# Optimization experiments

Hardware: AMD Instinct MI355X
Metric: run time of the kernel (lower is better)

Reference implementation:

```python
import jax, jax.numpy as jnp
import numpy as np

DIM = 512
HEADS = 8
DIM_HEAD = 64
INNER = HEADS * DIM_HEAD  # 512
EPS_LN = 1e-5
EPS_Q = 1e-6


def ternary_quant(w):
    # BitNet-style ternary quantization: scale by mean |w|, round to {-1,0,1}
    s = jnp.mean(jnp.abs(w))
    return jnp.round(jnp.clip(w / (s + EPS_Q), -1.0, 1.0)) * s


def layernorm(x, g, b):
    mu = jnp.mean(x, axis=-1, keepdims=True)
    var = jnp.mean(jnp.square(x - mu), axis=-1, keepdims=True)
    return (x - mu) * jax.lax.rsqrt(var + EPS_LN) * g + b


def setup_inputs() -> dict:
    key = jax.random.key(0)
    ks = jax.random.split(key, 6)
    x = jax.random.normal(ks[0], (8, 1024, DIM), dtype=jnp.float32)
    W_qkv = jax.random.normal(ks[1], (3 * INNER, DIM), dtype=jnp.float32) * (DIM ** -0.5)
    W_out = jax.random.normal(ks[2], (DIM, INNER), dtype=jnp.float32) * (INNER ** -0.5)
    b_out = jnp.zeros((DIM,), dtype=jnp.float32)
    g1 = jnp.ones((DIM,), dtype=jnp.float32)
    b1 = jnp.zeros((DIM,), dtype=jnp.float32)
    g2 = jnp.ones((INNER,), dtype=jnp.float32)
    b2 = jnp.zeros((INNER,), dtype=jnp.float32)
    return {"x": x, "g1": g1, "b1": b1, "W_qkv": W_qkv, "g2": g2, "b2": b2, "W_out": W_out, "b_out": b_out}


def reference(x, g1, b1, W_qkv, g2, b2, W_out, b_out):
    b, n, _ = x.shape
    scale = DIM_HEAD ** -0.5
    x = layernorm(x, g1, b1)
    qkv = x @ ternary_quant(W_qkv).T  # [b, n, 3*inner]
    q, k, v = jnp.split(qkv, 3, axis=-1)
    # b n (h d) -> b h n d
    def split_heads(t):
        return t.reshape(b, n, HEADS, DIM_HEAD).transpose(0, 2, 1, 3)
    q, k, v = split_heads(q), split_heads(k), split_heads(v)
    attn_map = jnp.einsum('bhnd,bhmd->bhnm', q, k) * scale  # [b,h,n,n]
    attn = jax.nn.softmax(attn_map, axis=-1)
    out = jnp.einsum('bhnm,bhmd->bhnd', attn, v)
    out = out.transpose(0, 2, 1, 3).reshape(b, n, INNER)  # b n (h d)
    out = layernorm(out, g2, b2)
    out = out @ ternary_quant(W_out).T + b_out
    return out
```

## Files before the change

### kernel.cpp

```cpp
#include <hip/hip_runtime.h>
#include <hip/hip_bf16.h>

typedef __bf16 bf16x8 __attribute__((ext_vector_type(8)));
typedef float  f32x4  __attribute__((ext_vector_type(4)));

#define SEQ   1024
#define BATCH 8
#define DIMM  512
#define HEADS 8
#define DHEAD 64
#define TRIPLE 1536
#define MROWS (BATCH*SEQ)

#define GLOAD_LDS16(g, l) __builtin_amdgcn_global_load_lds( \
    (const __attribute__((address_space(1))) void*)(const void*)(g), \
    (__attribute__((address_space(3))) void*)(void*)(l), 16, 0, 0)

__global__ __launch_bounds__(256) void absum_all(const float* __restrict__ w1,
                                                 const float* __restrict__ w2,
                                                 float* __restrict__ part) {
    const int bid = blockIdx.x, tid = threadIdx.x;
    float s = 0.f;
    if (bid < 256) {
        const float4* p = (const float4*)w1;
        for (int i = bid * 256 + tid; i < 196608; i += 65536) {
            float4 v = p[i];
            s += fabsf(v.x) + fabsf(v.y) + fabsf(v.z) + fabsf(v.w);
        }
    } else {
        const float4* p = (const float4*)w2;
        for (int i = (bid - 256) * 256 + tid; i < 65536; i += 16384) {
            float4 v = p[i];
            s += fabsf(v.x) + fabsf(v.y) + fabsf(v.z) + fabsf(v.w);
        }
    }
    for (int o = 32; o; o >>= 1) s += __shfl_down(s, o);
    __shared__ float red[4];
    if (!(tid & 63)) red[tid >> 6] = s;
    __syncthreads();
    if (tid == 0) part[bid] = red[0] + red[1] + red[2] + red[3];
}

__global__ __launch_bounds__(256) void quant_all(const float* __restrict__ w1,
                                                 const float* __restrict__ w2,
                                                 const float* __restrict__ part,
                                                 __bf16* __restrict__ o1,
                                                 __bf16* __restrict__ o2) {
    const int bid = blockIdx.x, tid = threadIdx.x;
    float acc = 0.f;
    if (bid < 768) acc = part[tid];
    else if (tid < 64) acc = part[256 + tid];
    for (int o = 32; o; o >>= 1) acc += __shfl_down(acc, o);
    __shared__ float red[4];
    if (!(tid & 63)) red[tid >> 6] = acc;
    __syncthreads();
    const float tot = red[0] + red[1] + red[2] + red[3];
    const float s = (bid < 768) ? tot / 786432.0f : tot / 262144.0f;
    const float inv = 1.f / (s + 1e-6f);

    const float* w; __bf16* o; int idx;
    if (bid < 768) { w = w1; o = o1; idx = (bid * 256 + tid) * 4; }
    else           { w = w2; o = o2; idx = ((bid - 768) * 256 + tid) * 4; }
    float4 v = *reinterpret_cast<const float4*>(w + idx);
    o[idx + 0] = (__bf16)(rintf(fminf(1.f, fmaxf(-1.f, v.x * inv))) * s);
    o[idx + 1] = (__bf16)(rintf(fminf(1.f, fmaxf(-1.f, v.y * inv))) * s);
    o[idx + 2] = (__bf16)(rintf(fminf(1.f, fmaxf(-1.f, v.z * inv))) * s);
    o[idx + 3] = (__bf16)(rintf(fminf(1.f, fmaxf(-1.f, v.w * inv))) * s);
}

template<typename TIN>
__global__ __launch_bounds__(256) void ln_fast(const TIN* __restrict__ x,
                                               const float* __restrict__ g,
                                               const float* __restrict__ bta,
                                               __bf16* __restrict__ y) {
    const int row = blockIdx.x * 4 + (threadIdx.x >> 6);
    const int lane = threadIdx.x & 63;
    float v[8];
    if constexpr (sizeof(TIN) == 4) {
        const float4* xr = (const float4*)((const float*)x + (size_t)row * DIMM + lane * 8);
        float4 a = xr[0], bq = xr[1];
        v[0] = a.x; v[1] = a.y; v[2] = a.z; v[3] = a.w;
        v[4] = bq.x; v[5] = bq.y; v[6] = bq.z; v[7] = bq.w;
    } else {
        bf16x8 a = *reinterpret_cast<const bf16x8*>((const __bf16*)x + (size_t)row * DIMM + lane * 8);
#pragma unroll
        for (int e = 0; e < 8; ++e) v[e] = (float)a[e];
    }
    float s = 0.f, sq = 0.f;
#pragma unroll
    for (int e = 0; e < 8; ++e) { s += v[e]; sq += v[e] * v[e]; }
    for (int o = 32; o; o >>= 1) { s += __shfl_xor(s, o); sq += __shfl_xor(sq, o); }
    const float mu = s * (1.f / DIMM);
    const float invs = rsqrtf(sq * (1.f / DIMM) - mu * mu + 1e-5f);
    const float4* gp = (const float4*)(g + lane * 8);
    const float4* bp = (const float4*)(bta + lane * 8);
    float4 g0 = gp[0], g1 = gp[1], b0 = bp[0], b1 = bp[1];
    float o_[8] = {
        (v[0] - mu) * invs * g0.x + b0.x, (v[1] - mu) * invs * g0.y + b0.y,
        (v[2] - mu) * invs * g0.z + b0.z, (v[3] - mu) * invs * g0.w + b0.w,
        (v[4] - mu) * invs * g1.x + b1.x, (v[5] - mu) * invs * g1.y + b1.y,
        (v[6] - mu) * invs * g1.z + b1.z, (v[7] - mu) * invs * g1.w + b1.w };
    uint4 st;
    asm("v_cvt_pk_bf16_f32 %0, %1, %2" : "=v"(st.x) : "v"(o_[0]), "v"(o_[1]));
    asm("v_cvt_pk_bf16_f32 %0, %1, %2" : "=v"(st.y) : "v"(o_[2]), "v"(o_[3]));
    asm("v_cvt_pk_bf16_f32 %0, %1, %2" : "=v"(st.z) : "v"(o_[4]), "v"(o_[5]));
    asm("v_cvt_pk_bf16_f32 %0, %1, %2" : "=v"(st.w) : "v"(o_[6]), "v"(o_[7]));
    *reinterpret_cast<uint4*>(y + (size_t)row * DIMM + lane * 8) = st;
}

template<int NCOLS, bool BIAS, bool OUT_F32>
__global__ __launch_bounds__(256) void gemm_lds(const __bf16* __restrict__ A,
                                                const __bf16* __restrict__ Wt,
                                                const float* __restrict__ bias,
                                                __bf16* __restrict__ outb,
                                                float* __restrict__ outf) {
    const int K = DIMM;
    __shared__ __align__(16) __bf16 As[2][4096];
    __shared__ __align__(16) __bf16 Bs[2][4096];

    const int tid = threadIdx.x;
    const int w = tid >> 6, lane = tid & 63;
    const int m = lane & 15, g = lane >> 4;
    const int mi = w >> 1, ni = w & 1;

    const int trow = tid >> 2;
    const int tc = tid & 3;
    const int sc = (tc ^ ((trow >> 1) & 3)) * 8;
    const __bf16* a0 = A  + (size_t)(blockIdx.x * 128 + trow) * K + sc;
    const __bf16* a1 = a0 + (size_t)64 * K;
    const __bf16* b0 = Wt + (size_t)(blockIdx.y * 128 + trow) * K + sc;
    const __bf16* b1 = b0 + (size_t)64 * K;

    f32x4 acc[4][4] = {};

    GLOAD_LDS16(a0, (char*)As[0] + tid * 16);
    GLOAD_LDS16(a1, (char*)As[0] + 4096 + tid * 16);
    GLOAD_LDS16(b0, (char*)Bs[0] + tid * 16);
    GLOAD_LDS16(b1, (char*)Bs[0] + 4096 + tid * 16);

    int cur = 0;
    for (int k0 = 0; k0 < K; k0 += 32) {
        __syncthreads();
        if (k0 + 32 < K) {
            GLOAD_LDS16(a0 + k0 + 32, (char*)As[cur ^ 1] + tid * 16);
            GLOAD_LDS16(a1 + k0 + 32, (char*)As[cur ^ 1] + 4096 + tid * 16);
            GLOAD_LDS16(b0 + k0 + 32, (char*)Bs[cur ^ 1] + tid * 16);
            GLOAD_LDS16(b1 + k0 + 32, (char*)Bs[cur ^ 1] + 4096 + tid * 16);
        }

        const char* Ab = (const char*)As[cur];
        const char* Bb = (const char*)Bs[cur];
        bf16x8 af[4], bfr[4];
#pragma unroll
        for (int i = 0; i < 4; ++i) {
            const int ra = mi * 64 + i * 16 + m;
            af[i] = *reinterpret_cast<const bf16x8*>(Ab + ra * 64 + ((g ^ ((ra >> 1) & 3)) << 4));
        }
#pragma unroll
        for (int j = 0; j < 4; ++j) {
            const int rb = ni * 64 + j * 16 + m;
            bfr[j] = *reinterpret_cast<const bf16x8*>(Bb + rb * 64 + ((g ^ ((rb >> 1) & 3)) << 4));
        }
#pragma unroll
        for (int i = 0; i < 4; ++i)
#pragma unroll
            for (int j = 0; j < 4; ++j)
                acc[i][j] = __builtin_amdgcn_mfma_f32_16x16x32_bf16(af[i], bfr[j], acc[i][j], 0, 0, 0);
        cur ^= 1;
    }

    const int orow0 = blockIdx.x * 128 + mi * 64 + g * 4;
    const int ocol0 = blockIdx.y * 128 + ni * 64;
#pragma unroll
    for (int i = 0; i < 4; ++i)
#pragma unroll
        for (int j = 0; j < 4; ++j)
#pragma unroll
            for (int r = 0; r < 4; ++r) {
                int row = orow0 + i * 16 + r;
                int col = ocol0 + j * 16 + m;
                float v = acc[i][j][r];
                if (BIAS) v += bias[col];
                if (OUT_F32) outf[(size_t)row * NCOLS + col] = v;
                else         outb[(size_t)row * NCOLS + col] = (__bf16)v;
            }
}

__global__ __launch_bounds__(256) void transpose_v(const __bf16* __restrict__ qkv,
                                                   __bf16* __restrict__ vtg) {
    __shared__ __align__(16) __bf16 Vl[4096];
    const int bh = blockIdx.x, nt = blockIdx.y;
    const int b = bh >> 3, h = bh & 7;
    const int tid = threadIdx.x;
    const int r = tid >> 3, c = tid & 7;
    const __bf16* src = qkv + (size_t)(b * SEQ + nt * 64 + r) * TRIPLE + 2 * DIMM + h * 64 + c * 8;
    uint4 v0 = *reinterpret_cast<const uint4*>(src);
    uint4 v1 = *reinterpret_cast<const uint4*>(src + (size_t)32 * TRIPLE);
    char* lp = (char*)Vl;
    *reinterpret_cast<uint4*>(lp + r * 128 + ((c ^ (r & 7)) << 4)) = v0;
    *reinterpret_cast<uint4*>(lp + (r + 32) * 128 + ((c ^ (r & 7)) << 4)) = v1;
    __syncthreads();
    const int d = tid >> 2, qtr = tid & 3;
    const int cd = d >> 3, dby = (d & 7) * 2;
    unsigned un[8];
#pragma unroll
    for (int s2 = 0; s2 < 8; ++s2) {
        const int tok0 = qtr * 16 + s2 * 2, tok1 = tok0 + 1;
        unsigned lo = *reinterpret_cast<const unsigned short*>(lp + tok0 * 128 + ((cd ^ (tok0 & 7)) << 4) + dby);
        unsigned hi = *reinterpret_cast<const unsigned short*>(lp + tok1 * 128 + ((cd ^ (tok1 & 7)) << 4) + dby);
        un[s2] = lo | (hi << 16);
    }
    __bf16* dst = vtg + (size_t)(bh * 64 + d) * SEQ + nt * 64 + qtr * 16;
    *reinterpret_cast<uint4*>(dst)     = make_uint4(un[0], un[1], un[2], un[3]);
    *reinterpret_cast<uint4*>(dst + 8) = make_uint4(un[4], un[5], un[6], un[7]);
}

__global__ __launch_bounds__(256, 4) void attn_mfma(const __bf16* __restrict__ qkv,
                                                    const __bf16* __restrict__ vtg,
                                                    __bf16* __restrict__ out) {
    const int bh = blockIdx.x, qt = blockIdx.y;
    const int b = bh >> 3, h = bh & 7;
    const int tid = threadIdx.x;
    const int w = tid >> 6, lane = tid & 63;
    const int g = lane >> 4, m = lane & 15;

    __shared__ __align__(16) __bf16 Kb[2][4096];
    __shared__ __align__(16) __bf16 Vb[2][4096];
    __shared__ __align__(16) __bf16 Pl[4][1024];

    bf16x8 qf[2];
    {
        const __bf16* qp = qkv + (size_t)(b * SEQ + qt * 64 + w * 16 + m) * TRIPLE + h * 64 + g * 8;
        qf[0] = *reinterpret_cast<const bf16x8*>(qp);
        qf[1] = *reinterpret_cast<const bf16x8*>(qp + 32);
#pragma unroll
        for (int e = 0; e < 8; ++e) {
            qf[0][e] = (__bf16)((float)qf[0][e] * 0.125f);
            qf[1][e] = (__bf16)((float)qf[1][e] * 0.125f);
        }
    }

    const int sr = tid >> 3;
    const int sp = tid & 7;
    const int scn = sp ^ (sr & 7);
    const __bf16* ksrc = qkv + (size_t)(b * SEQ + sr) * TRIPLE + DIMM + h * 64 + scn * 8;
    const __bf16* vsrc = vtg + (size_t)(bh * 64 + sr) * SEQ + scn * 8;
    const size_t kstep = (size_t)64 * TRIPLE;

    auto stage = [&](int bb, int t) {
        GLOAD_LDS16(ksrc + (size_t)t * kstep,                       (char*)Kb[bb] + tid * 16);
        GLOAD_LDS16(ksrc + (size_t)t * kstep + (size_t)32 * TRIPLE, (char*)Kb[bb] + 4096 + tid * 16);
        GLOAD_LDS16(vsrc + t * 64,                                  (char*)Vb[bb] + tid * 16);
        GLOAD_LDS16(vsrc + t * 64 + (size_t)32 * SEQ,               (char*)Vb[bb] + 4096 + tid * 16);
    };

    f32x4 oa[4] = {};
    float mrun = -1e30f, lrun = 0.f;
    char* pw = (char*)Pl[w] + m * 128;
    const int psw = (m & 7) << 4;

    stage(0, 0);
    int cur = 0;
    for (int t = 0; t < 16; ++t) {
        __syncthreads();
        if (t < 15) stage(cur ^ 1, t + 1);

        const char* kb = (const char*)Kb[cur];
        const char* vb = (const char*)Vb[cur];

        f32x4 sa[4];
#pragma unroll
        for (int i = 0; i < 4; ++i) sa[i] = (f32x4){0.f, 0.f, 0.f, 0.f};
#pragma unroll
        for (int kc = 0; kc < 2; ++kc) {
            const int cp = ((kc * 4 + g) ^ (m & 7)) << 4;
#pragma unroll
            for (int i = 0; i < 4; ++i) {
                bf16x8 kf = *reinterpret_cast<const bf16x8*>(kb + (i * 16 + m) * 128 + cp);
                sa[i] = __builtin_amdgcn_mfma_f32_16x16x32_bf16(kf, qf[kc], sa[i], 0, 0, 0);
            }
        }

        {
            float mx = -1e30f;
#pragma unroll
            for (int i = 0; i < 4; ++i)
#pragma unroll
                for (int r = 0; r < 4; ++r) mx = fmaxf(mx, sa[i][r]);
            mx = fmaxf(mx, __shfl_xor(mx, 16));
            mx = fmaxf(mx, __shfl_xor(mx, 32));
            const float mnew = fmaxf(mrun, mx);
            float p[4][4];
            float ps = 0.f;
#pragma unroll
            for (int i = 0; i < 4; ++i)
#pragma unroll
                for (int r = 0; r < 4; ++r) { p[i][r] = __expf(sa[i][r] - mnew); ps += p[i][r]; }
            ps += __shfl_xor(ps, 16);
            ps += __shfl_xor(ps, 32);
            const float al = __expf(mrun - mnew);
            mrun = mnew;
            lrun = lrun * al + ps;
#pragma unroll
            for (int i = 0; i < 4; ++i)
#pragma unroll
                for (int r = 0; r < 4; ++r) oa[i][r] *= al;
#pragma unroll
            for (int i = 0; i < 4; ++i) {
                uint2 pk;
                asm("v_cvt_pk_bf16_f32 %0, %1, %2" : "=v"(pk.x) : "v"(p[i][0]), "v"(p[i][1]));
                asm("v_cvt_pk_bf16_f32 %0, %1, %2" : "=v"(pk.y) : "v"(p[i][2]), "v"(p[i][3]));
                *reinterpret_cast<uint2*>(pw + ((i * 32 + g * 8) ^ psw)) = pk;
            }
        }

        bf16x8 pf[2];
#pragma unroll
        for (int kc = 0; kc < 2; ++kc)
            pf[kc] = *reinterpret_cast<const bf16x8*>(pw + ((kc * 64 + g * 16) ^ psw));

#pragma unroll
        for (int kc = 0; kc < 2; ++kc) {
            const int cp = ((kc * 4 + g) ^ (m & 7)) << 4;
#pragma unroll
            for (int i = 0; i < 4; ++i) {
                bf16x8 vf = *reinterpret_cast<const bf16x8*>(vb + (i * 16 + m) * 128 + cp);
                oa[i] = __builtin_amdgcn_mfma_f32_16x16x32_bf16(vf, pf[kc], oa[i], 0, 0, 0);
            }
        }

        cur ^= 1;
    }

    const float inv = 1.0f / lrun;
    unsigned int* orow = (unsigned int*)(out +
        (size_t)(b * SEQ + qt * 64 + w * 16 + m) * DIMM + h * 64);
#pragma unroll
    for (int i = 0; i < 4; ++i)
#pragma unroll
        for (int rp = 0; rp < 2; ++rp) {
            float o0 = oa[i][2 * rp] * inv, o1 = oa[i][2 * rp + 1] * inv;
            unsigned int pk;
            asm("v_cvt_pk_bf16_f32 %0, %1, %2" : "=v"(pk) : "v"(o0), "v"(o1));
            orow[i * 8 + g * 2 + rp] = pk;
        }
}

extern "C" void kernel_launch(void* const* d_in, const int* in_sizes, int n_in,
                              void* d_out, int out_size, void* d_ws, size_t ws_size,
                              hipStream_t stream) {
    const float* x     = (const float*)d_in[0];
    const float* g1    = (const float*)d_in[1];
    const float* b1    = (const float*)d_in[2];
    const float* W_qkv = (const float*)d_in[3];
    const float* g2    = (const float*)d_in[4];
    const float* b2    = (const float*)d_in[5];
    const float* W_out = (const float*)d_in[6];
    const float* b_out = (const float*)d_in[7];
    float* out = (float*)d_out;

    char* ws = (char*)d_ws;
    float* part   = (float*)(ws);
    __bf16* Wq1 = (__bf16*)(ws + 4096);
    __bf16* Wq2 = (__bf16*)(ws + 4096 + 1572864);
    __bf16* Xln = (__bf16*)(ws + 4096 + 1572864 + 524288);
    __bf16* QKV = (__bf16*)(ws + 4096 + 1572864 + 524288 + 8388608);
    __bf16* AO  = (__bf16*)(ws + 4096 + 1572864 + 524288 + 8388608 + 25165824);
    __bf16* VT  = Xln;

    absum_all<<<320, 256, 0, stream>>>(W_qkv, W_out, part);
    quant_all<<<1024, 256, 0, stream>>>(W_qkv, W_out, part, Wq1, Wq2);
    ln_fast<float><<<MROWS / 4, 256, 0, stream>>>(x, g1, b1, Xln);
    gemm_lds<TRIPLE, false, false><<<dim3(64, 12), 256, 0, stream>>>(Xln, Wq1, nullptr, QKV, nullptr);
    transpose_v<<<dim3(64, 16), 256, 0, stream>>>(QKV, VT);
    attn_mfma<<<dim3(64, 16), 256, 0, stream>>>(QKV, VT, AO);
    ln_fast<__bf16><<<MROWS / 4, 256, 0, stream>>>(AO, g2, b2, Xln);
    gemm_lds<DIMM, true, true><<<dim3(64, 4), 256, 0, stream>>>(Xln, Wq2, b_out, nullptr, out);
}
```

Baseline: 93.28 us.

## Process 128 query rows per attention block to reuse K/V tiles twice

The attention kernel now gives each wave 32 query rows (two 16-row halves) instead of 16, so each block covers 128 queries and the grid's query dimension halves. Each K/V fragment loaded from LDS feeds two MFMAs, which halves K/V global staging and LDS reads per query. In exchange, register use roughly doubles (launch bounds relaxed from 4 to 2 blocks per SM), the P scratch buffer doubles, and there are half as many blocks (512) to spread across the CUs.

```diff
diff --git a/kernel.cpp b/kernel.cpp
--- a/kernel.cpp
+++ b/kernel.cpp
@@ -215,7 +215,7 @@
     *reinterpret_cast<uint4*>(dst + 8) = make_uint4(un[4], un[5], un[6], un[7]);
 }
 
-__global__ __launch_bounds__(256, 4) void attn_mfma(const __bf16* __restrict__ qkv,
+__global__ __launch_bounds__(256, 2) void attn_mfma(const __bf16* __restrict__ qkv,
                                                     const __bf16* __restrict__ vtg,
                                                     __bf16* __restrict__ out) {
     const int bh = blockIdx.x, qt = blockIdx.y;
@@ -226,17 +226,20 @@
 
     __shared__ __align__(16) __bf16 Kb[2][4096];
     __shared__ __align__(16) __bf16 Vb[2][4096];
-    __shared__ __align__(16) __bf16 Pl[4][1024];
-
-    bf16x8 qf[2];
+    __shared__ __align__(16) __bf16 Pl[4][2048];
+
+    bf16x8 qf[2][2];
     {
-        const __bf16* qp = qkv + (size_t)(b * SEQ + qt * 64 + w * 16 + m) * TRIPLE + h * 64 + g * 8;
-        qf[0] = *reinterpret_cast<const bf16x8*>(qp);
-        qf[1] = *reinterpret_cast<const bf16x8*>(qp + 32);
-#pragma unroll
-        for (int e = 0; e < 8; ++e) {
-            qf[0][e] = (__bf16)((float)qf[0][e] * 0.125f);
-            qf[1][e] = (__bf16)((float)qf[1][e] * 0.125f);
+        const __bf16* qp = qkv + (size_t)(b * SEQ + qt * 128 + w * 32 + m) * TRIPLE + h * 64 + g * 8;
+#pragma unroll
+        for (int hf = 0; hf < 2; ++hf) {
+            qf[hf][0] = *reinterpret_cast<const bf16x8*>(qp + (size_t)hf * 16 * TRIPLE);
+            qf[hf][1] = *reinterpret_cast<const bf16x8*>(qp + (size_t)hf * 16 * TRIPLE + 32);
+#pragma unroll
+            for (int e = 0; e < 8; ++e) {
+                qf[hf][0][e] = (__bf16)((float)qf[hf][0][e] * 0.125f);
+                qf[hf][1][e] = (__bf16)((float)qf[hf][1][e] * 0.125f);
+            }
         }
     }
 
@@ -254,8 +257,8 @@
         GLOAD_LDS16(vsrc + t * 64 + (size_t)32 * SEQ,               (char*)Vb[bb] + 4096 + tid * 16);
     };
 
-    f32x4 oa[4] = {};
-    float mrun = -1e30f, lrun = 0.f;
+    f32x4 oa[2][4] = {};
+    float mrun[2] = {-1e30f, -1e30f}, lrun[2] = {0.f, 0.f};
     char* pw = (char*)Pl[w] + m * 128;
     const int psw = (m & 7) << 4;
 
@@ -268,56 +271,63 @@
         const char* kb = (const char*)Kb[cur];
         const char* vb = (const char*)Vb[cur];
 
-        f32x4 sa[4];
-#pragma unroll
-        for (int i = 0; i < 4; ++i) sa[i] = (f32x4){0.f, 0.f, 0.f, 0.f};
+        f32x4 sa[2][4];
+#pragma unroll
+        for (int hf = 0; hf < 2; ++hf)
+#pragma unroll
+            for (int i = 0; i < 4; ++i) sa[hf][i] = (f32x4){0.f, 0.f, 0.f, 0.f};
 #pragma unroll
         for (int kc = 0; kc < 2; ++kc) {
             const int cp = ((kc * 4 + g) ^ (m & 7)) << 4;
 #pragma unroll
             for (int i = 0; i < 4; ++i) {
                 bf16x8 kf = *reinterpret_cast<const bf16x8*>(kb + (i * 16 + m) * 128 + cp);
-                sa[i] = __builtin_amdgcn_mfma_f32_16x16x32_bf16(kf, qf[kc], sa[i], 0, 0, 0);
-            }
-        }
-
-        {
+                sa[0][i] = __builtin_amdgcn_mfma_f32_16x16x32_bf16(kf, qf[0][kc], sa[0][i], 0, 0, 0);
+                sa[1][i] = __builtin_amdgcn_mfma_f32_16x16x32_bf16(kf, qf[1][kc], sa[1][i], 0, 0, 0);
+            }
+        }
+
+#pragma unroll
+        for (int hf = 0; hf < 2; ++hf) {
             float mx = -1e30f;
 #pragma unroll
             for (int i = 0; i < 4; ++i)
 #pragma unroll
-                for (int r = 0; r < 4; ++r) mx = fmaxf(mx, sa[i][r]);
+                for (int r = 0; r < 4; ++r) mx = fmaxf(mx, sa[hf][i][r]);
             mx = fmaxf(mx, __shfl_xor(mx, 16));
             mx = fmaxf(mx, __shfl_xor(mx, 32));
-            const float mnew = fmaxf(mrun, mx);
+            const float mnew = fmaxf(mrun[hf], mx);
             float p[4][4];
             float ps = 0.f;
 #pragma unroll
             for (int i = 0; i < 4; ++i)
 #pragma unroll
-                for (int r = 0; r < 4; ++r) { p[i][r] = __expf(sa[i][r] - mnew); ps += p[i][r]; }
+                for (int r = 0; r < 4; ++r) { p[i][r] = __expf(sa[hf][i][r] - mnew); ps += p[i][r]; }
             ps += __shfl_xor(ps, 16);
             ps += __shfl_xor(ps, 32);
-            const float al = __expf(mrun - mnew);
-            mrun = mnew;
-            lrun = lrun * al + ps;
+            const float al = __expf(mrun[hf] - mnew);
+            mrun[hf] = mnew;
+            lrun[hf] = lrun[hf] * al + ps;
 #pragma unroll
             for (int i = 0; i < 4; ++i)
 #pragma unroll
-                for (int r = 0; r < 4; ++r) oa[i][r] *= al;
+                for (int r = 0; r < 4; ++r) oa[hf][i][r] *= al;
 #pragma unroll
             for (int i = 0; i < 4; ++i) {
                 uint2 pk;
                 asm("v_cvt_pk_bf16_f32 %0, %1, %2" : "=v"(pk.x) : "v"(p[i][0]), "v"(p[i][1]));
                 asm("v_cvt_pk_bf16_f32 %0, %1, %2" : "=v"(pk.y) : "v"(p[i][2]), "v"(p[i][3]));
-                *reinterpret_cast<uint2*>(pw + ((i * 32 + g * 8) ^ psw)) = pk;
-            }
-        }
-
-        bf16x8 pf[2];
-#pragma unroll
-        for (int kc = 0; kc < 2; ++kc)
-            pf[kc] = *reinterpret_cast<const bf16x8*>(pw + ((kc * 64 + g * 16) ^ psw));
+                *reinterpret_cast<uint2*>(pw + hf * 16 * 128 + ((i * 32 + g * 8) ^ psw)) = pk;
+            }
+        }
+
+        bf16x8 pf[2][2];
+#pragma unroll
+        for (int hf = 0; hf < 2; ++hf)
+#pragma unroll
+            for (int kc = 0; kc < 2; ++kc)
+                pf[hf][kc] = *reinterpret_cast<const bf16x8*>(
+                    pw + hf * 16 * 128 + ((kc * 64 + g * 16) ^ psw));
 
 #pragma unroll
         for (int kc = 0; kc < 2; ++kc) {
@@ -325,25 +335,29 @@
 #pragma unroll
             for (int i = 0; i < 4; ++i) {
                 bf16x8 vf = *reinterpret_cast<const bf16x8*>(vb + (i * 16 + m) * 128 + cp);
-                oa[i] = __builtin_amdgcn_mfma_f32_16x16x32_bf16(vf, pf[kc], oa[i], 0, 0, 0);
+                oa[0][i] = __builtin_amdgcn_mfma_f32_16x16x32_bf16(vf, pf[0][kc], oa[0][i], 0, 0, 0);
+                oa[1][i] = __builtin_amdgcn_mfma_f32_16x16x32_bf16(vf, pf[1][kc], oa[1][i], 0, 0, 0);
             }
         }
 
         cur ^= 1;
     }
 
-    const float inv = 1.0f / lrun;
-    unsigned int* orow = (unsigned int*)(out +
-        (size_t)(b * SEQ + qt * 64 + w * 16 + m) * DIMM + h * 64);
-#pragma unroll
-    for (int i = 0; i < 4; ++i)
-#pragma unroll
-        for (int rp = 0; rp < 2; ++rp) {
-            float o0 = oa[i][2 * rp] * inv, o1 = oa[i][2 * rp + 1] * inv;
-            unsigned int pk;
-            asm("v_cvt_pk_bf16_f32 %0, %1, %2" : "=v"(pk) : "v"(o0), "v"(o1));
-            orow[i * 8 + g * 2 + rp] = pk;
-        }
+#pragma unroll
+    for (int hf = 0; hf < 2; ++hf) {
+        const float inv = 1.0f / lrun[hf];
+        unsigned int* orow = (unsigned int*)(out +
+            (size_t)(b * SEQ + qt * 128 + w * 32 + hf * 16 + m) * DIMM + h * 64);
+#pragma unroll
+        for (int i = 0; i < 4; ++i)
+#pragma unroll
+            for (int rp = 0; rp < 2; ++rp) {
+                float o0 = oa[hf][i][2 * rp] * inv, o1 = oa[hf][i][2 * rp + 1] * inv;
+                unsigned int pk;
+                asm("v_cvt_pk_bf16_f32 %0, %1, %2" : "=v"(pk) : "v"(o0), "v"(o1));
+                orow[i * 8 + g * 2 + rp] = pk;
+            }
+    }
 }
 
 extern "C" void kernel_launch(void* const* d_in, const int* in_sizes, int n_in,
@@ -373,7 +387,7 @@
     ln_fast<float><<<MROWS / 4, 256, 0, stream>>>(x, g1, b1, Xln);
     gemm_lds<TRIPLE, false, false><<<dim3(64, 12), 256, 0, stream>>>(Xln, Wq1, nullptr, QKV, nullptr);
     transpose_v<<<dim3(64, 16), 256, 0, stream>>>(QKV, VT);
-    attn_mfma<<<dim3(64, 16), 256, 0, stream>>>(QKV, VT, AO);
+    attn_mfma<<<dim3(64, 8), 256, 0, stream>>>(QKV, VT, AO);
     ln_fast<__bf16><<<MROWS / 4, 256, 0, stream>>>(AO, g2, b2, Xln);
     gemm_lds<DIMM, true, true><<<dim3(64, 4), 256, 0, stream>>>(Xln, Wq2, b_out, nullptr, out);
 }
```

Result: no change. 93.75 us (+0.5%).

## Fuse weight quant with first layernorm and write V transposed from QKV GEMM

Applied to the files above, without the earlier changes.

Merges the weight quantization kernel and the input layernorm into one launch, using the block index to pick the work. Removes the separate V transpose kernel by having the QKV GEMM epilogue write Q/K into a 1024-wide buffer and V directly in transposed [b,h,d,n] layout. This saves two launches and one full read/write pass of V. The transposed V stores from the GEMM epilogue are scattered 2-byte writes with a stride of 1024 elements, so that epilogue may become costlier.

```diff
diff --git a/kernel.cpp b/kernel.cpp
--- a/kernel.cpp
+++ b/kernel.cpp
@@ -41,31 +41,62 @@
     if (tid == 0) part[bid] = red[0] + red[1] + red[2] + red[3];
 }
 
-__global__ __launch_bounds__(256) void quant_all(const float* __restrict__ w1,
-                                                 const float* __restrict__ w2,
-                                                 const float* __restrict__ part,
-                                                 __bf16* __restrict__ o1,
-                                                 __bf16* __restrict__ o2) {
+__global__ __launch_bounds__(256) void quant_ln(const float* __restrict__ w1,
+                                                const float* __restrict__ w2,
+                                                const float* __restrict__ part,
+                                                const float* __restrict__ x,
+                                                const float* __restrict__ g1,
+                                                const float* __restrict__ b1,
+                                                __bf16* __restrict__ o1,
+                                                __bf16* __restrict__ o2,
+                                                __bf16* __restrict__ y) {
     const int bid = blockIdx.x, tid = threadIdx.x;
-    float acc = 0.f;
-    if (bid < 768) acc = part[tid];
-    else if (tid < 64) acc = part[256 + tid];
-    for (int o = 32; o; o >>= 1) acc += __shfl_down(acc, o);
-    __shared__ float red[4];
-    if (!(tid & 63)) red[tid >> 6] = acc;
-    __syncthreads();
-    const float tot = red[0] + red[1] + red[2] + red[3];
-    const float s = (bid < 768) ? tot / 786432.0f : tot / 262144.0f;
-    const float inv = 1.f / (s + 1e-6f);
-
-    const float* w; __bf16* o; int idx;
-    if (bid < 768) { w = w1; o = o1; idx = (bid * 256 + tid) * 4; }
-    else           { w = w2; o = o2; idx = ((bid - 768) * 256 + tid) * 4; }
-    float4 v = *reinterpret_cast<const float4*>(w + idx);
-    o[idx + 0] = (__bf16)(rintf(fminf(1.f, fmaxf(-1.f, v.x * inv))) * s);
-    o[idx + 1] = (__bf16)(rintf(fminf(1.f, fmaxf(-1.f, v.y * inv))) * s);
-    o[idx + 2] = (__bf16)(rintf(fminf(1.f, fmaxf(-1.f, v.z * inv))) * s);
-    o[idx + 3] = (__bf16)(rintf(fminf(1.f, fmaxf(-1.f, v.w * inv))) * s);
+    if (bid < 1024) {
+        float acc = 0.f;
+        if (bid < 768) acc = part[tid];
+        else if (tid < 64) acc = part[256 + tid];
+        for (int o = 32; o; o >>= 1) acc += __shfl_down(acc, o);
+        __shared__ float red[4];
+        if (!(tid & 63)) red[tid >> 6] = acc;
+        __syncthreads();
+        const float tot = red[0] + red[1] + red[2] + red[3];
+        const float s = (bid < 768) ? tot / 786432.0f : tot / 262144.0f;
+        const float inv = 1.f / (s + 1e-6f);
+        const float* w; __bf16* o; int idx;
+        if (bid < 768) { w = w1; o = o1; idx = (bid * 256 + tid) * 4; }
+        else           { w = w2; o = o2; idx = ((bid - 768) * 256 + tid) * 4; }
+        float4 v = *reinterpret_cast<const float4*>(w + idx);
+        o[idx + 0] = (__bf16)(rintf(fminf(1.f, fmaxf(-1.f, v.x * inv))) * s);
+        o[idx + 1] = (__bf16)(rintf(fminf(1.f, fmaxf(-1.f, v.y * inv))) * s);
+        o[idx + 2] = (__bf16)(rintf(fminf(1.f, fmaxf(-1.f, v.z * inv))) * s);
+        o[idx + 3] = (__bf16)(rintf(fminf(1.f, fmaxf(-1.f, v.w * inv))) * s);
+    } else {
+        const int row = (bid - 1024) * 4 + (tid >> 6);
+        const int lane = tid & 63;
+        const float4* xr = (const float4*)(x + (size_t)row * DIMM + lane * 8);
+        float4 a = xr[0], bq = xr[1];
+        float v[8] = {a.x, a.y, a.z, a.w, bq.x, bq.y, bq.z, bq.w};
+        float s = 0.f, sq = 0.f;
+#pragma unroll
+        for (int e = 0; e < 8; ++e) { s += v[e]; sq += v[e] * v[e]; }
+        for (int o = 32; o; o >>= 1) { s += __shfl_xor(s, o); sq += __shfl_xor(sq, o); }
+        const float mu = s * (1.f / DIMM);
+        const float invs = rsqrtf(sq * (1.f / DIMM) - mu * mu + 1e-5f);
+        const float4* gp = (const float4*)(g1 + lane * 8);
+        const float4* bp = (const float4*)(b1 + lane * 8);
+        float4 g0 = gp[0], g1v = gp[1], b0 = bp[0], b1v = bp[1];
+        float o_[8] = {
+            (v[0] - mu) * invs * g0.x + b0.x, (v[1] - mu) * invs * g0.y + b0.y,
+            (v[2] - mu) * invs * g0.z + b0.z, (v[3] - mu) * invs * g0.w + b0.w,
+            (v[4] - mu) * invs * g1v.x + b1v.x, (v[5] - mu) * invs * g1v.y + b1v.y,
+            (v[6] - mu) * invs * g1v.z + b1v.z, (v[7] - mu) * invs * g1v.w + b1v.w };
+        uint4 st;
+        asm("v_cvt_pk_bf16_f32 %0, %1, %2" : "=v"(st.x) : "v"(o_[0]), "v"(o_[1]));
+        asm("v_cvt_pk_bf16_f32 %0, %1, %2" : "=v"(st.y) : "v"(o_[2]), "v"(o_[3]));
+        asm("v_cvt_pk_bf16_f32 %0, %1, %2" : "=v"(st.z) : "v"(o_[4]), "v"(o_[5]));
+        asm("v_cvt_pk_bf16_f32 %0, %1, %2" : "=v"(st.w) : "v"(o_[6]), "v"(o_[7]));
+        *reinterpret_cast<uint4*>(y + (size_t)row * DIMM + lane * 8) = st;
+    }
 }
 
 template<typename TIN>
@@ -108,12 +139,13 @@
     *reinterpret_cast<uint4*>(y + (size_t)row * DIMM + lane * 8) = st;
 }
 
-template<int NCOLS, bool BIAS, bool OUT_F32>
+template<int NCOLS, bool BIAS, bool OUT_F32, bool VSPLIT>
 __global__ __launch_bounds__(256) void gemm_lds(const __bf16* __restrict__ A,
                                                 const __bf16* __restrict__ Wt,
                                                 const float* __restrict__ bias,
                                                 __bf16* __restrict__ outb,
-                                                float* __restrict__ outf) {
+                                                float* __restrict__ outf,
+                                                __bf16* __restrict__ vt) {
     const int K = DIMM;
     __shared__ __align__(16) __bf16 As[2][4096];
     __shared__ __align__(16) __bf16 Bs[2][4096];
@@ -181,41 +213,23 @@
                 int col = ocol0 + j * 16 + m;
                 float v = acc[i][j][r];
                 if (BIAS) v += bias[col];
-                if (OUT_F32) outf[(size_t)row * NCOLS + col] = v;
-                else         outb[(size_t)row * NCOLS + col] = (__bf16)v;
+                if (VSPLIT) {
+                    if (col < 1024) {
+                        outb[(size_t)row * 1024 + col] = (__bf16)v;
+                    } else {
+                        const int vc = col - 1024;
+                        vt[(size_t)(((row >> 10) * 8 + (vc >> 6)) * 64 + (vc & 63)) * 1024
+                           + (row & 1023)] = (__bf16)v;
+                    }
+                } else if (OUT_F32) {
+                    outf[(size_t)row * NCOLS + col] = v;
+                } else {
+                    outb[(size_t)row * NCOLS + col] = (__bf16)v;
+                }
             }
 }
 
-__global__ __launch_bounds__(256) void transpose_v(const __bf16* __restrict__ qkv,
-                                                   __bf16* __restrict__ vtg) {
-    __shared__ __align__(16) __bf16 Vl[4096];
-    const int bh = blockIdx.x, nt = blockIdx.y;
-    const int b = bh >> 3, h = bh & 7;
-    const int tid = threadIdx.x;
-    const int r = tid >> 3, c = tid & 7;
-    const __bf16* src = qkv + (size_t)(b * SEQ + nt * 64 + r) * TRIPLE + 2 * DIMM + h * 64 + c * 8;
-    uint4 v0 = *reinterpret_cast<const uint4*>(src);
-    uint4 v1 = *reinterpret_cast<const uint4*>(src + (size_t)32 * TRIPLE);
-    char* lp = (char*)Vl;
-    *reinterpret_cast<uint4*>(lp + r * 128 + ((c ^ (r & 7)) << 4)) = v0;
-    *reinterpret_cast<uint4*>(lp + (r + 32) * 128 + ((c ^ (r & 7)) << 4)) = v1;
-    __syncthreads();
-    const int d = tid >> 2, qtr = tid & 3;
-    const int cd = d >> 3, dby = (d & 7) * 2;
-    unsigned un[8];
-#pragma unroll
-    for (int s2 = 0; s2 < 8; ++s2) {
-        const int tok0 = qtr * 16 + s2 * 2, tok1 = tok0 + 1;
-        unsigned lo = *reinterpret_cast<const unsigned short*>(lp + tok0 * 128 + ((cd ^ (tok0 & 7)) << 4) + dby);
-        unsigned hi = *reinterpret_cast<const unsigned short*>(lp + tok1 * 128 + ((cd ^ (tok1 & 7)) << 4) + dby);
-        un[s2] = lo | (hi << 16);
-    }
-    __bf16* dst = vtg + (size_t)(bh * 64 + d) * SEQ + nt * 64 + qtr * 16;
-    *reinterpret_cast<uint4*>(dst)     = make_uint4(un[0], un[1], un[2], un[3]);
-    *reinterpret_cast<uint4*>(dst + 8) = make_uint4(un[4], un[5], un[6], un[7]);
-}
-
-__global__ __launch_bounds__(256, 4) void attn_mfma(const __bf16* __restrict__ qkv,
+__global__ __launch_bounds__(256, 4) void attn_mfma(const __bf16* __restrict__ qk,
                                                     const __bf16* __restrict__ vtg,
                                                     __bf16* __restrict__ out) {
     const int bh = blockIdx.x, qt = blockIdx.y;
@@ -230,7 +244,7 @@
 
     bf16x8 qf[2];
     {
-        const __bf16* qp = qkv + (size_t)(b * SEQ + qt * 64 + w * 16 + m) * TRIPLE + h * 64 + g * 8;
+        const __bf16* qp = qk + (size_t)(b * SEQ + qt * 64 + w * 16 + m) * 1024 + h * 64 + g * 8;
         qf[0] = *reinterpret_cast<const bf16x8*>(qp);
         qf[1] = *reinterpret_cast<const bf16x8*>(qp + 32);
 #pragma unroll
@@ -243,15 +257,15 @@
     const int sr = tid >> 3;
     const int sp = tid & 7;
     const int scn = sp ^ (sr & 7);
-    const __bf16* ksrc = qkv + (size_t)(b * SEQ + sr) * TRIPLE + DIMM + h * 64 + scn * 8;
+    const __bf16* ksrc = qk + (size_t)(b * SEQ + sr) * 1024 + 512 + h * 64 + scn * 8;
     const __bf16* vsrc = vtg + (size_t)(bh * 64 + sr) * SEQ + scn * 8;
-    const size_t kstep = (size_t)64 * TRIPLE;
+    const size_t kstep = (size_t)64 * 1024;
 
     auto stage = [&](int bb, int t) {
-        GLOAD_LDS16(ksrc + (size_t)t * kstep,                       (char*)Kb[bb] + tid * 16);
-        GLOAD_LDS16(ksrc + (size_t)t * kstep + (size_t)32 * TRIPLE, (char*)Kb[bb] + 4096 + tid * 16);
-        GLOAD_LDS16(vsrc + t * 64,                                  (char*)Vb[bb] + tid * 16);
-        GLOAD_LDS16(vsrc + t * 64 + (size_t)32 * SEQ,               (char*)Vb[bb] + 4096 + tid * 16);
+        GLOAD_LDS16(ksrc + (size_t)t * kstep,                      (char*)Kb[bb] + tid * 16);
+        GLOAD_LDS16(ksrc + (size_t)t * kstep + (size_t)32 * 1024,  (char*)Kb[bb] + 4096 + tid * 16);
+        GLOAD_LDS16(vsrc + t * 64,                                 (char*)Vb[bb] + tid * 16);
+        GLOAD_LDS16(vsrc + t * 64 + (size_t)32 * SEQ,              (char*)Vb[bb] + 4096 + tid * 16);
     };
 
     f32x4 oa[4] = {};
@@ -363,17 +377,15 @@
     float* part   = (float*)(ws);
     __bf16* Wq1 = (__bf16*)(ws + 4096);
     __bf16* Wq2 = (__bf16*)(ws + 4096 + 1572864);
-    __bf16* Xln = (__bf16*)(ws + 4096 + 1572864 + 524288);
-    __bf16* QKV = (__bf16*)(ws + 4096 + 1572864 + 524288 + 8388608);
-    __bf16* AO  = (__bf16*)(ws + 4096 + 1572864 + 524288 + 8388608 + 25165824);
-    __bf16* VT  = Xln;
+    __bf16* Xln = (__bf16*)(ws + 2101248);
+    __bf16* QK  = (__bf16*)(ws + 10489856);
+    __bf16* VT  = (__bf16*)(ws + 27267072);
+    __bf16* AO  = (__bf16*)(ws + 35655680);
 
     absum_all<<<320, 256, 0, stream>>>(W_qkv, W_out, part);
-    quant_all<<<1024, 256, 0, stream>>>(W_qkv, W_out, part, Wq1, Wq2);
-    ln_fast<float><<<MROWS / 4, 256, 0, stream>>>(x, g1, b1, Xln);
-    gemm_lds<TRIPLE, false, false><<<dim3(64, 12), 256, 0, stream>>>(Xln, Wq1, nullptr, QKV, nullptr);
-    transpose_v<<<dim3(64, 16), 256, 0, stream>>>(QKV, VT);
-    attn_mfma<<<dim3(64, 16), 256, 0, stream>>>(QKV, VT, AO);
+    quant_ln<<<3072, 256, 0, stream>>>(W_qkv, W_out, part, x, g1, b1, Wq1, Wq2, Xln);
+    gemm_lds<TRIPLE, false, false, true><<<dim3(64, 12), 256, 0, stream>>>(Xln, Wq1, nullptr, QK, nullptr, VT);
+    attn_mfma<<<dim3(64, 16), 256, 0, stream>>>(QK, VT, AO);
     ln_fast<__bf16><<<MROWS / 4, 256, 0, stream>>>(AO, g2, b2, Xln);
-    gemm_lds<DIMM, true, true><<<dim3(64, 4), 256, 0, stream>>>(Xln, Wq2, b_out, nullptr, out);
-}
+    gemm_lds<DIMM, true, true, false><<<dim3(64, 4), 256, 0, stream>>>(Xln, Wq2, b_out, nullptr, out, nullptr);
+}
```

Measured after the change: 93.06 us. About the same (-0.2%).
